# Kernel optimization log

Measured on AMD Instinct MI355X. Metric: run time of the kernel, lower is better.

## Reference

```python
import jax, jax.numpy as jnp
import numpy as np

B, S, N_ITEMS, E, H, L, DFF = 32, 512, 2048, 512, 8, 2, 2048
DK = E // H
EPS = 1e-5


def setup_inputs() -> dict:
    key = jax.random.key(0)
    ks = jax.random.split(key, 32)
    sc = 0.02
    p = {
        'input_seq': jax.random.normal(ks[0], (B, S, N_ITEMS), jnp.float32),
        'emb_W': jax.random.normal(ks[1], (N_ITEMS, E), jnp.float32) * sc,
        'emb_b': jnp.zeros((E,), jnp.float32),
        'pos_emb': jax.random.normal(ks[2], (S, E), jnp.float32) * sc,
        'Wq': jax.random.normal(ks[3], (L, E, E), jnp.float32) * sc,
        'bq': jnp.zeros((L, E), jnp.float32),
        'Wk': jax.random.normal(ks[4], (L, E, E), jnp.float32) * sc,
        'bk': jnp.zeros((L, E), jnp.float32),
        'Wv': jax.random.normal(ks[5], (L, E, E), jnp.float32) * sc,
        'bv': jnp.zeros((L, E), jnp.float32),
        'Wo': jax.random.normal(ks[6], (L, E, E), jnp.float32) * sc,
        'bo': jnp.zeros((L, E), jnp.float32),
        'ln1_g': jnp.ones((L, E), jnp.float32),
        'ln1_b': jnp.zeros((L, E), jnp.float32),
        'W1': jax.random.normal(ks[7], (L, E, DFF), jnp.float32) * sc,
        'b1': jnp.zeros((L, DFF), jnp.float32),
        'W2': jax.random.normal(ks[8], (L, DFF, E), jnp.float32) * sc,
        'b2': jnp.zeros((L, E), jnp.float32),
        'ln2_g': jnp.ones((L, E), jnp.float32),
        'ln2_b': jnp.zeros((L, E), jnp.float32),
        'fc_W': jax.random.normal(ks[9], (E, 1), jnp.float32) * sc,
        'fc_b': jnp.zeros((1,), jnp.float32),
    }
    return p


def _layernorm(x, g, b):
    m = jnp.mean(x, axis=-1, keepdims=True)
    v = jnp.mean(jnp.square(x - m), axis=-1, keepdims=True)
    return (x - m) * jax.lax.rsqrt(v + EPS) * g + b


def reference(input_seq, emb_W, emb_b, pos_emb, Wq, bq, Wk, bk, Wv, bv, Wo, bo,
              ln1_g, ln1_b, W1, b1, W2, b2, ln2_g, ln2_b, fc_W, fc_b):
    x = input_seq @ emb_W + emb_b          # [B,S,E]
    x = x + pos_emb[None, :, :]
    tril = jnp.tril(jnp.ones((S, S), jnp.float32))  # causal lower-triangular
    for l in range(L):
        # --- self attention (faithful: tril BEFORE scale, zeros not -inf) ---
        q = (x @ Wq[l] + bq[l]).reshape(B, S, H, DK).transpose(0, 2, 1, 3)
        k = (x @ Wk[l] + bk[l]).reshape(B, S, H, DK).transpose(0, 2, 1, 3)
        v = (x @ Wv[l] + bv[l]).reshape(B, S, H, DK).transpose(0, 2, 1, 3)
        scores = jnp.einsum('bhqd,bhkd->bhqk', q, k)
        scores = (scores * tril) / np.sqrt(DK)
        probs = jax.nn.softmax(scores, axis=-1)
        attn = jnp.einsum('bhqk,bhkd->bhqd', probs, v)  # [B,H,S,DK]
        attn = attn.transpose(0, 2, 1, 3).reshape(B, S, E)
        attn = attn @ Wo[l] + bo[l]
        # faithful source bug: `self_attention(x,x,x)[0]` -> batch 0 only,
        # broadcast over all batches in the residual add
        attended0 = attn[0]                 # [S,E]
        x = _layernorm(x + attended0[None, :, :], ln1_g[l], ln1_b[l])
        # --- feed forward ---
        ff = jax.nn.relu(x @ W1[l] + b1[l]) @ W2[l] + b2[l]
        x = _layernorm(x + ff, ln2_g[l], ln2_b[l])
    out = (x @ fc_W + fc_b).squeeze(-1)     # [B,S]
    return out
```

## Files before the change

kernel.cpp:

```cpp
#include <hip/hip_runtime.h>


typedef __bf16 bf16;
typedef __bf16 bf16x8 __attribute__((ext_vector_type(8)));
typedef __bf16 bf16x4 __attribute__((ext_vector_type(4)));
typedef float  f32x4  __attribute__((ext_vector_type(4)));

#define SEQ 512

__device__ __forceinline__ void gl2lds16(const bf16* g, void* l) {
    __builtin_amdgcn_global_load_lds(
        (const __attribute__((address_space(1))) void*)g,
        (__attribute__((address_space(3))) void*)l, 16, 0, 0);
}

template<int N> __device__ __forceinline__ void waitvm() {
    if constexpr (N == 0)      asm volatile("s_waitcnt vmcnt(0)" ::: "memory");
    else if constexpr (N == 2) asm volatile("s_waitcnt vmcnt(2)" ::: "memory");
    else if constexpr (N == 3) asm volatile("s_waitcnt vmcnt(3)" ::: "memory");
    else if constexpr (N == 4) asm volatile("s_waitcnt vmcnt(4)" ::: "memory");
    else if constexpr (N == 5) asm volatile("s_waitcnt vmcnt(5)" ::: "memory");
    else if constexpr (N == 6) asm volatile("s_waitcnt vmcnt(6)" ::: "memory");
    else if constexpr (N == 8) asm volatile("s_waitcnt vmcnt(8)" ::: "memory");
    else static_assert(N == 0, "unsupported waitvm");
}

__global__ __launch_bounds__(256)
void cvt_k(const float* __restrict__ in, bf16* __restrict__ outb)
{
    const long long gsz = (long long)gridDim.x * 256;
    const long long n8 = 16384ll * 2048 / 8;
    long long i = (long long)blockIdx.x * 256 + threadIdx.x;
    for (; i + 3 * gsz < n8; i += 4 * gsz) {
        f32x4 a0 = *(const f32x4*)(in + i * 8);
        f32x4 b0 = *(const f32x4*)(in + i * 8 + 4);
        f32x4 a1 = *(const f32x4*)(in + (i + gsz) * 8);
        f32x4 b1 = *(const f32x4*)(in + (i + gsz) * 8 + 4);
        f32x4 a2 = *(const f32x4*)(in + (i + 2 * gsz) * 8);
        f32x4 b2 = *(const f32x4*)(in + (i + 2 * gsz) * 8 + 4);
        f32x4 a3 = *(const f32x4*)(in + (i + 3 * gsz) * 8);
        f32x4 b3 = *(const f32x4*)(in + (i + 3 * gsz) * 8 + 4);
        bf16x8 w0, w1, w2, w3;
        #pragma unroll
        for (int j = 0; j < 4; ++j) {
            w0[j] = (bf16)a0[j]; w0[4 + j] = (bf16)b0[j];
            w1[j] = (bf16)a1[j]; w1[4 + j] = (bf16)b1[j];
            w2[j] = (bf16)a2[j]; w2[4 + j] = (bf16)b2[j];
            w3[j] = (bf16)a3[j]; w3[4 + j] = (bf16)b3[j];
        }
        *(bf16x8*)(outb + i * 8)             = w0;
        *(bf16x8*)(outb + (i + gsz) * 8)     = w1;
        *(bf16x8*)(outb + (i + 2 * gsz) * 8) = w2;
        *(bf16x8*)(outb + (i + 3 * gsz) * 8) = w3;
    }
    for (; i < n8; i += gsz) {
        f32x4 a0 = *(const f32x4*)(in + i * 8);
        f32x4 b0 = *(const f32x4*)(in + i * 8 + 4);
        bf16x8 w0;
        #pragma unroll
        for (int j = 0; j < 4; ++j) { w0[j] = (bf16)a0[j]; w0[4 + j] = (bf16)b0[j]; }
        *(bf16x8*)(outb + i * 8) = w0;
    }
}

__global__ __launch_bounds__(256)
void wtall_k(const float* __restrict__ emb_W, bf16* __restrict__ embWT,
             const float* __restrict__ Wq, const float* __restrict__ Wk,
             const float* __restrict__ Wv, const float* __restrict__ Wo,
             const float* __restrict__ W1, const float* __restrict__ W2,
             bf16* __restrict__ qkvWT, bf16* __restrict__ WoT,
             bf16* __restrict__ W1T, bf16* __restrict__ W2T,
             const float* __restrict__ bq, const float* __restrict__ bk,
             const float* __restrict__ bv, float* __restrict__ qkvB)
{
    const int b = blockIdx.x;
    if (b < 7168) {
        const float* src;
        bf16* dst;
        int K, N, t;
        if (b < 1024) {
            src = emb_W; dst = embWT; K = 2048; N = 512; t = b;
        } else {
            const int bb = b - 1024;
            const int l = bb >= 3072 ? 1 : 0;
            const int r = bb - l * 3072;
            if (r < 256)       { src = Wq + l * 262144;  dst = qkvWT + l * 786432;          K = 512;  N = 512;  t = r; }
            else if (r < 512)  { src = Wk + l * 262144;  dst = qkvWT + l * 786432 + 262144; K = 512;  N = 512;  t = r - 256; }
            else if (r < 768)  { src = Wv + l * 262144;  dst = qkvWT + l * 786432 + 524288; K = 512;  N = 512;  t = r - 512; }
            else if (r < 1024) { src = Wo + l * 262144;  dst = WoT + l * 262144;            K = 512;  N = 512;  t = r - 768; }
            else if (r < 2048) { src = W1 + l * 1048576; dst = W1T + l * 1048576;           K = 512;  N = 2048; t = r - 1024; }
            else               { src = W2 + l * 1048576; dst = W2T + l * 1048576;           K = 2048; N = 512;  t = r - 2048; }
        }
        const int tx = N >> 5;
        const int n0 = (t % tx) * 32, k0 = (t / tx) * 32;
        __shared__ float tl[32][33];
        int r2 = threadIdx.x >> 3, c4 = (threadIdx.x & 7) * 4;
        float4 v = *(const float4*)&src[(long long)(k0 + r2) * N + n0 + c4];
        tl[r2][c4 + 0] = v.x; tl[r2][c4 + 1] = v.y;
        tl[r2][c4 + 2] = v.z; tl[r2][c4 + 3] = v.w;
        __syncthreads();
        int n = threadIdx.x >> 3, kk4 = (threadIdx.x & 7) * 4;
        bf16x4 o;
        o[0] = (bf16)tl[kk4 + 0][n]; o[1] = (bf16)tl[kk4 + 1][n];
        o[2] = (bf16)tl[kk4 + 2][n]; o[3] = (bf16)tl[kk4 + 3][n];
        *(bf16x4*)&dst[(long long)(n0 + n) * K + k0 + kk4] = o;
    } else {
        const int l = b - 7168;
        for (int t2 = threadIdx.x; t2 < 512; t2 += 256) {
            qkvB[l * 1536 + t2]        = bq[l * 512 + t2];
            qkvB[l * 1536 + 512 + t2]  = bk[l * 512 + t2];
            qkvB[l * 1536 + 1024 + t2] = bv[l * 512 + t2];
        }
    }
}

__global__ __launch_bounds__(512, 1)
void fattn(const bf16* __restrict__ qkv,
           const bf16* __restrict__ VT,
           bf16* __restrict__ attn0b)
{
    __shared__ __align__(1024) char smem[65536 + 65536 + 8192];
    char* Ks = smem;
    char* Vs = smem + 65536;
    const int h = blockIdx.y;
    const int q0 = blockIdx.x * 128;
    const int tid = threadIdx.x, lane = tid & 63, wv = tid >> 6;
    const int fr = lane & 15, fc = lane >> 4;
    char* Ps = smem + 131072 + wv * 1024;

    {
        const bf16* Kg = qkv + 512 + h * 64;
        #pragma unroll
        for (int p = 0; p < 8; ++p) {
            int row = p * 64 + (tid >> 3);
            int ch  = tid & 7;
            gl2lds16(Kg + (long long)row * 1536 + ((ch ^ (row & 7)) * 8),
                     Ks + p * 8192 + tid * 16);
        }
        const bf16* Vg = VT + (long long)h * 64 * 512;
        #pragma unroll
        for (int p = 0; p < 8; ++p) {
            int row = p * 8 + (tid >> 6);
            int ch  = tid & 63;
            int chg = (ch & ~7) | ((ch & 7) ^ (row & 7));
            gl2lds16(Vg + (long long)row * 512 + chg * 8,
                     Vs + p * 8192 + tid * 16);
        }
    }
    const int q0w = q0 + wv * 16;
    const int qg  = q0w + fr;
    bf16x8 qf[2];
    #pragma unroll
    for (int w = 0; w < 2; ++w)
        qf[w] = *(const bf16x8*)(qkv + (long long)qg * 1536 + h * 64 + w * 32 + fc * 8);

    asm volatile("s_waitcnt vmcnt(0)" ::: "memory");
    __builtin_amdgcn_s_barrier();
    asm volatile("" ::: "memory");

    f32x4 s[32] = {};
    #pragma unroll
    for (int kt = 0; kt < 32; ++kt) {
        #pragma unroll
        for (int w = 0; w < 2; ++w) {
            int row = kt * 16 + fr;
            bf16x8 kf = *(const bf16x8*)(Ks + row * 128 +
                                         (((w * 4 + fc) ^ (row & 7)) * 16));
            s[kt] = __builtin_amdgcn_mfma_f32_16x16x32_bf16(kf, qf[w], s[kt], 0, 0, 0);
        }
    }

    float mx = -3.4e38f;
    #pragma unroll
    for (int kt = 0; kt < 32; ++kt)
        #pragma unroll
        for (int rr = 0; rr < 4; ++rr) {
            int k = kt * 16 + fc * 4 + rr;
            float v = (k <= qg) ? s[kt][rr] * 0.125f : 0.0f;
            s[kt][rr] = v;
            mx = fmaxf(mx, v);
        }
    mx = fmaxf(mx, __shfl_xor(mx, 16));
    mx = fmaxf(mx, __shfl_xor(mx, 32));
    float sum = 0.f;
    #pragma unroll
    for (int kt = 0; kt < 32; ++kt)
        #pragma unroll
        for (int rr = 0; rr < 4; ++rr) {
            float e = __expf(s[kt][rr] - mx);
            s[kt][rr] = e;
            sum += e;
        }
    sum += __shfl_xor(sum, 16);
    sum += __shfl_xor(sum, 32);
    const float inv = 1.0f / sum;

    f32x4 o[4] = {};
    #pragma unroll
    for (int kt2 = 0; kt2 < 16; ++kt2) {
        bf16x4 u0, u1;
        #pragma unroll
        for (int rr = 0; rr < 4; ++rr) {
            u0[rr] = (bf16)(s[2 * kt2][rr] * inv);
            u1[rr] = (bf16)(s[2 * kt2 + 1][rr] * inv);
        }
        *(bf16x4*)(Ps + fr * 64 + ((fc ^ (fr & 7)) * 8))       = u0;
        *(bf16x4*)(Ps + fr * 64 + (((4 + fc) ^ (fr & 7)) * 8)) = u1;
        __threadfence_block();
        bf16x4 lo = *(const bf16x4*)(Ps + fr * 64 + (((2 * fc) ^ (fr & 7)) * 8));
        bf16x4 hi = *(const bf16x4*)(Ps + fr * 64 + (((2 * fc + 1) ^ (fr & 7)) * 8));
        bf16x8 pf;
        pf[0] = lo[0]; pf[1] = lo[1]; pf[2] = lo[2]; pf[3] = lo[3];
        pf[4] = hi[0]; pf[5] = hi[1]; pf[6] = hi[2]; pf[7] = hi[3];
        #pragma unroll
        for (int n = 0; n < 4; ++n) {
            int row = n * 16 + fr;
            int ch  = kt2 * 4 + fc;
            int chs = (ch & ~7) | ((ch & 7) ^ (row & 7));
            bf16x8 vf = *(const bf16x8*)(Vs + row * 1024 + chs * 16);
            o[n] = __builtin_amdgcn_mfma_f32_16x16x32_bf16(pf, vf, o[n], 0, 0, 0);
        }
    }

    #pragma unroll
    for (int n = 0; n < 4; ++n)
        #pragma unroll
        for (int rr = 0; rr < 4; ++rr) {
            int qrow = q0w + fc * 4 + rr;
            attn0b[(long long)qrow * 512 + h * 64 + n * 16 + fr] = (bf16)o[n][rr];
        }
}

template<int BN, int ACT, int POS>
__global__ __launch_bounds__(512, 1)
void mg8(const bf16* __restrict__ Ab, int lda,
         const bf16* __restrict__ Bt, int ldb,
         const float* __restrict__ bias, const float* __restrict__ pos,
         bf16* __restrict__ Cb, int ldc, int K)
{
    constexpr int BM = 256;
    constexpr int APASS = 2;
    constexpr int BPASS = BN / 128;
    constexpr int AHB = BM * 64;
    constexpr int BHB = BN * 64;
    constexpr int WM = (BN == 256 ? 2 : 4), WN = 8 / WM;
    constexpr int MR = BM / WM / 16;
    constexpr int NR = BN / WN / 16;
    __shared__ __align__(1024) char smem[4 * AHB + 4 * BHB];
    char* ABase = smem;
    char* BBase = smem + 4 * AHB;

    const int gx = gridDim.x, gy = gridDim.y;
    const int nwg = gx * gy;
    const int b = blockIdx.y * gx + blockIdx.x;
    const int q = nwg >> 3, r = nwg & 7;
    const int xcd = b & 7, loc = b >> 3;
    const int wg = (xcd < r ? xcd * (q + 1) : r * (q + 1) + (xcd - r) * q) + loc;
    const int bx = wg % gx, by = wg / gx;
    const int row0 = by * BM, col0 = bx * BN;

    const int tid = threadIdx.x, lane = tid & 63, wv = tid >> 6;
    const int wr = (WM == 2 ? (wv >> 2) : (wv >> 1));
    const int wc = (WM == 2 ? (wv & 3) : (wv & 1));
    const int fr = lane & 15, fc = lane >> 4;

    const bf16* aS[APASS];
    #pragma unroll
    for (int p = 0; p < APASS; ++p) {
        int cL = p * 512 + tid;
        int row = cL >> 2, ch = cL & 3;
        aS[p] = Ab + (long long)(row0 + row) * lda + ((ch ^ (row & 3)) * 8);
    }
    const bf16* bS[BPASS];
    #pragma unroll
    for (int p = 0; p < BPASS; ++p) {
        int cL = p * 512 + tid;
        int row = cL >> 2, ch = cL & 3;
        bS[p] = Bt + (long long)(col0 + row) * ldb + ((ch ^ (row & 3)) * 8);
    }
    int aOff[MR], bOff[NR];
    #pragma unroll
    for (int m = 0; m < MR; ++m) {
        int row = wr * (BM / WM) + m * 16 + fr;
        aOff[m] = row * 64 + ((fc ^ (row & 3)) * 16);
    }
    #pragma unroll
    for (int n = 0; n < NR; ++n) {
        int row = wc * (BN / WN) + n * 16 + fr;
        bOff[n] = row * 64 + ((fc ^ (row & 3)) * 16);
    }

    auto stagePart = [&](int j) {
        const int tau = j >> 2, kh = (j >> 1) & 1, d = tau & 1;
        const int koff = tau * 64 + kh * 32;
        if (!(j & 1)) {
            char* dst = ABase + (d * 2 + kh) * AHB + wv * 1024;
            #pragma unroll
            for (int p = 0; p < APASS; ++p)
                gl2lds16(aS[p] + koff, dst + p * 8192);
        } else {
            char* dst = BBase + (d * 2 + kh) * BHB + wv * 1024;
            #pragma unroll
            for (int p = 0; p < BPASS; ++p)
                gl2lds16(bS[p] + koff, dst + p * 8192);
        }
    };

    const int nt = K >> 6;
    const int T = 4 * nt;
    #pragma unroll
    for (int j = 0; j < 6; ++j)
        if (j < T) stagePart(j);
    waitvm<2 * (APASS + BPASS)>();
    __builtin_amdgcn_s_barrier();

    f32x4 acc[MR][NR] = {};
    const int NPH = 2 * nt;
    for (int g = 0; g < NPH; ++g) {
        const int tau = g >> 1, ks = g & 1, d = tau & 1;

        const char* as = ABase + (d * 2 + ks) * AHB;
        const char* bs = BBase + (d * 2 + ks) * BHB;
        bf16x8 a[MR], b2[NR];
        #pragma unroll
        for (int m = 0; m < MR; ++m) a[m] = *(const bf16x8*)(as + aOff[m]);
        #pragma unroll
        for (int n = 0; n < NR; ++n) b2[n] = *(const bf16x8*)(bs + bOff[n]);

        if (2 * g + 6 < T) stagePart(2 * g + 6);
        if (2 * g + 7 < T) stagePart(2 * g + 7);

        __builtin_amdgcn_s_setprio(1);
        #pragma unroll
        for (int m = 0; m < MR; ++m)
            #pragma unroll
            for (int n = 0; n < NR; ++n)
                acc[m][n] = __builtin_amdgcn_mfma_f32_16x16x32_bf16(
                    a[m], b2[n], acc[m][n], 0, 0, 0);
        __builtin_amdgcn_s_setprio(0);

        const int rem = T - (2 * g + 4);
        if (rem >= 4)      waitvm<2 * (APASS + BPASS)>();
        else if (rem == 3) waitvm<2 * APASS + BPASS>();
        else if (rem == 2) waitvm<APASS + BPASS>();
        else if (rem == 1) waitvm<APASS>();
        else               waitvm<0>();
        __builtin_amdgcn_s_barrier();
    }

    float* st = (float*)(smem + wv * 4096);
    const int rowb = row0 + wr * (BM / WM);
    const int colb = col0 + wc * (BN / WN);
    #pragma unroll
    for (int m = 0; m < MR; ++m) {
        #pragma unroll
        for (int n = 0; n < NR; ++n) {
            int col = colb + n * 16 + fr;
            float bb = bias ? bias[col] : 0.f;
            #pragma unroll
            for (int rr = 0; rr < 4; ++rr) {
                float x = acc[m][n][rr] + bb;
                if constexpr (POS) {
                    int rowg = rowb + m * 16 + fc * 4 + rr;
                    x += pos[(rowg & 511) * 512 + col];
                }
                if constexpr (ACT) x = fmaxf(x, 0.f);
                st[(fc * 4 + rr) * 64 + n * 16 + fr] = x;
            }
        }
        #pragma unroll
        for (int sgi = 0; sgi < 2; ++sgi) {
            int row = sgi * 8 + (lane >> 3);
            int c8 = (lane & 7) * 8;
            f32x4 u = *(const f32x4*)&st[row * 64 + c8];
            f32x4 v = *(const f32x4*)&st[row * 64 + c8 + 4];
            bf16x8 w8;
            w8[0] = (bf16)u[0]; w8[1] = (bf16)u[1];
            w8[2] = (bf16)u[2]; w8[3] = (bf16)u[3];
            w8[4] = (bf16)v[0]; w8[5] = (bf16)v[1];
            w8[6] = (bf16)v[2]; w8[7] = (bf16)v[3];
            *(bf16x8*)&Cb[(long long)(rowb + m * 16 + row) * ldc + colb + c8] = w8;
        }
    }
}

template<int BM, int BN, int ACT, int CMODE, int CAUSAL>
__global__ __launch_bounds__(256, 4)
void mgemm(const bf16* __restrict__ Ab, int lda, long long sA,
           const bf16* __restrict__ Bt, int ldb, long long sB,
           const float* __restrict__ bias,
           float* __restrict__ Cf, bf16* __restrict__ Cb, int ldc, long long sC,
           int K)
{
    static_assert(BM == 128 && (BN == 128 || BN == 64), "tile");
    const int gx = gridDim.x, gy = gridDim.y;
    const int nwg = gx * gy;
    const int b = blockIdx.y * gx + blockIdx.x;
    const int q = nwg >> 3, r = nwg & 7;
    const int xcd = b & 7, loc = b >> 3;
    const int wg = (xcd < r ? xcd * (q + 1) : r * (q + 1) + (xcd - r) * q) + loc;
    const int bx = wg % gx, by = wg / gx;
    if (CAUSAL && bx * BN > by * BM + (BM - 1)) return;

    constexpr int TM = BM / 32, TN = BN / 32;
    constexpr int AIT = BM / 64, BIT = BN / 64;
    constexpr int ABY = BM * 64;
    constexpr int BBY = BN * 64;
    __shared__ bf16 As[2 * BM * 32];
    __shared__ bf16 Bs[2 * BN * 32];
    char* AsB = (char*)As;
    char* BsB = (char*)Bs;
    const int tid = threadIdx.x;
    const int lane = tid & 63, wv = tid >> 6;
    const int wr = wv >> 1, wc = wv & 1;
    const int fr = lane & 15, fc = lane >> 4;
    const int row0 = by * BM, col0 = bx * BN;
    const int z = blockIdx.z;

    Ab += (long long)z * sA;
    Bt += (long long)z * sB;
    if constexpr (CMODE == 0) Cf += (long long)z * sC;
    else                      Cb += (long long)z * sC;

    f32x4 acc[TM][TN] = {};

    const bf16* aSrc[AIT];
    #pragma unroll
    for (int it = 0; it < AIT; ++it) {
        int cL = it * 256 + tid;
        int row = cL >> 2, ch = cL & 3;
        aSrc[it] = Ab + (long long)(row0 + row) * lda + ((ch ^ (row & 3)) * 8);
    }
    const bf16* bSrc[BIT];
    #pragma unroll
    for (int it = 0; it < BIT; ++it) {
        int cL = it * 256 + tid;
        int row = cL >> 2, ch = cL & 3;
        bSrc[it] = Bt + (long long)(col0 + row) * ldb + ((ch ^ (row & 3)) * 8);
    }
    int aOff[TM], bOff[TN];
    #pragma unroll
    for (int m = 0; m < TM; ++m) {
        int row = wr * (BM / 2) + m * 16 + fr;
        aOff[m] = row * 64 + ((fc ^ (row & 3)) * 16);
    }
    #pragma unroll
    for (int n = 0; n < TN; ++n) {
        int row = wc * (BN / 2) + n * 16 + fr;
        bOff[n] = row * 64 + ((fc ^ (row & 3)) * 16);
    }

    auto stageTo = [&](int buf, int kt) {
        #pragma unroll
        for (int it = 0; it < AIT; ++it)
            gl2lds16(aSrc[it] + kt, AsB + buf * ABY + it * 4096 + wv * 1024);
        #pragma unroll
        for (int it = 0; it < BIT; ++it)
            gl2lds16(bSrc[it] + kt, BsB + buf * BBY + it * 4096 + wv * 1024);
    };

    const int nt = K >> 5;
    stageTo(0, 0);
    asm volatile("s_waitcnt vmcnt(0)" ::: "memory");
    __builtin_amdgcn_s_barrier();
    asm volatile("" ::: "memory");

    int cur = 0;
    for (int t = 0; t < nt; ++t) {
        if (t + 1 < nt) stageTo(cur ^ 1, (t + 1) * 32);
        bf16x8 a[TM], b2[TN];
        #pragma unroll
        for (int m = 0; m < TM; ++m) a[m] = *(const bf16x8*)(AsB + cur * ABY + aOff[m]);
        #pragma unroll
        for (int n = 0; n < TN; ++n) b2[n] = *(const bf16x8*)(BsB + cur * BBY + bOff[n]);
        __builtin_amdgcn_s_setprio(1);
        #pragma unroll
        for (int m = 0; m < TM; ++m)
            #pragma unroll
            for (int n = 0; n < TN; ++n)
                acc[m][n] = __builtin_amdgcn_mfma_f32_16x16x32_bf16(a[m], b2[n], acc[m][n], 0, 0, 0);
        __builtin_amdgcn_s_setprio(0);
        if (t + 1 < nt) {
            asm volatile("s_waitcnt vmcnt(0)" ::: "memory");
            __builtin_amdgcn_s_barrier();
            asm volatile("" ::: "memory");
            cur ^= 1;
        }
    }

    #pragma unroll
    for (int n = 0; n < TN; ++n) {
        int col = col0 + wc * (BN / 2) + n * 16 + fr;
        float bb = bias ? bias[col] : 0.f;
        #pragma unroll
        for (int m = 0; m < TM; ++m) {
            int rbase = row0 + wr * (BM / 2) + m * 16 + fc * 4;
            #pragma unroll
            for (int rr = 0; rr < 4; ++rr) {
                float x = acc[m][n][rr] + bb;
                if constexpr (ACT) x = fmaxf(x, 0.f);
                long long ci = (long long)(rbase + rr) * ldc + col;
                if constexpr (CMODE == 0) Cf[ci] = x;
                else                      Cb[ci] = (bf16)x;
            }
        }
    }
}

__global__ __launch_bounds__(256)
void vt_k(const bf16* __restrict__ qkv, bf16* __restrict__ VT)
{
    __shared__ bf16 t[64][80];
    int h = blockIdx.y, s0 = blockIdx.x * 64;
    int r = threadIdx.x >> 2, c16 = (threadIdx.x & 3) * 16;
    const bf16* src = qkv + (long long)(s0 + r) * 1536 + 1024 + h * 64 + c16;
    *(bf16x8*)&t[r][c16]     = *(const bf16x8*)src;
    *(bf16x8*)&t[r][c16 + 8] = *(const bf16x8*)(src + 8);
    __syncthreads();
    int d = r, seg = c16;
    bf16 tmp[16];
    #pragma unroll
    for (int j = 0; j < 16; ++j) tmp[j] = t[seg + j][d];
    bf16* dst = VT + ((long long)(h * 64 + d)) * 512 + s0 + seg;
    *(bf16x8*)dst       = *(bf16x8*)&tmp[0];
    *(bf16x8*)(dst + 8) = *(bf16x8*)&tmp[8];
}

__global__ __launch_bounds__(128)
void addln_k(bf16* __restrict__ xb, const bf16* __restrict__ res,
             unsigned resMask, const float* __restrict__ g,
             const float* __restrict__ bta)
{
    long long row = blockIdx.x;
    int tid = threadIdx.x;
    int c = tid * 4;
    bf16x4 xv4 = *(const bf16x4*)&xb[row * 512 + c];
    bf16x4 rv4 = *(const bf16x4*)&res[(long long)(blockIdx.x & resMask) * 512 + c];
    float x0 = (float)xv4[0] + (float)rv4[0];
    float x1 = (float)xv4[1] + (float)rv4[1];
    float x2 = (float)xv4[2] + (float)rv4[2];
    float x3 = (float)xv4[3] + (float)rv4[3];
    float s = x0 + x1 + x2 + x3;
    float qq = x0 * x0 + x1 * x1 + x2 * x2 + x3 * x3;
    #pragma unroll
    for (int off = 32; off; off >>= 1) {
        s += __shfl_xor(s, off);
        qq += __shfl_xor(qq, off);
    }
    __shared__ float rs[2], rq[2];
    if ((tid & 63) == 0) { rs[tid >> 6] = s; rq[tid >> 6] = qq; }
    __syncthreads();
    s = rs[0] + rs[1]; qq = rq[0] + rq[1];
    float mean = s * (1.0f / 512.0f);
    float var  = qq * (1.0f / 512.0f) - mean * mean;
    float rstd = rsqrtf(var + 1e-5f);
    float4 gv = *(const float4*)&g[c];
    float4 bv = *(const float4*)&bta[c];
    bf16x4 o4;
    o4[0] = (bf16)((x0 - mean) * rstd * gv.x + bv.x);
    o4[1] = (bf16)((x1 - mean) * rstd * gv.y + bv.y);
    o4[2] = (bf16)((x2 - mean) * rstd * gv.z + bv.z);
    o4[3] = (bf16)((x3 - mean) * rstd * gv.w + bv.w);
    *(bf16x4*)&xb[row * 512 + c] = o4;
}

__global__ __launch_bounds__(256)
void fc_k(const bf16* __restrict__ x, const float* __restrict__ w,
          const float* __restrict__ bb, float* __restrict__ out)
{
    int row  = blockIdx.x * 4 + (threadIdx.x >> 6);
    int lane = threadIdx.x & 63;
    const bf16* xr = x + (long long)row * 512;
    bf16x8 a8 = *(const bf16x8*)&xr[lane * 8];
    float4 w0 = *(const float4*)&w[lane * 8];
    float4 w1 = *(const float4*)&w[lane * 8 + 4];
    float s = (float)a8[0] * w0.x + (float)a8[1] * w0.y
            + (float)a8[2] * w0.z + (float)a8[3] * w0.w
            + (float)a8[4] * w1.x + (float)a8[5] * w1.y
            + (float)a8[6] * w1.z + (float)a8[7] * w1.w;
    #pragma unroll
    for (int off = 32; off; off >>= 1) s += __shfl_xor(s, off);
    if (lane == 0) out[row] = s + bb[0];
}

extern "C" void kernel_launch(void* const* d_in, const int* in_sizes, int n_in,
                              void* d_out, int out_size, void* d_ws, size_t ws_size,
                              hipStream_t stream)
{
    const float* input_seq = (const float*)d_in[0];
    const float* emb_W  = (const float*)d_in[1];
    const float* emb_b  = (const float*)d_in[2];
    const float* pos_emb= (const float*)d_in[3];
    const float* Wq = (const float*)d_in[4];
    const float* bq = (const float*)d_in[5];
    const float* Wk = (const float*)d_in[6];
    const float* bk = (const float*)d_in[7];
    const float* Wv = (const float*)d_in[8];
    const float* bv = (const float*)d_in[9];
    const float* Wo = (const float*)d_in[10];
    const float* bo = (const float*)d_in[11];
    const float* ln1_g = (const float*)d_in[12];
    const float* ln1_b = (const float*)d_in[13];
    const float* W1 = (const float*)d_in[14];
    const float* b1 = (const float*)d_in[15];
    const float* W2 = (const float*)d_in[16];
    const float* b2 = (const float*)d_in[17];
    const float* ln2_g = (const float*)d_in[18];
    const float* ln2_b = (const float*)d_in[19];
    const float* fcW = (const float*)d_in[20];
    const float* fcb = (const float*)d_in[21];
    float* out = (float*)d_out;

    char* w = (char*)d_ws;
    size_t off = 0;
    auto alloc = [&](size_t bytes) -> void* {
        off = (off + 255) & ~(size_t)255;
        void* p = w + off;
        off += bytes;
        return p;
    };
    bf16*  xb     = (bf16*) alloc(16384ull * 512 * 2);
    bf16*  embWT  = (bf16*) alloc(512ull * 2048 * 2);
    bf16*  qkvWT  = (bf16*) alloc(2ull * 1536 * 512 * 2);
    bf16*  WoT    = (bf16*) alloc(2ull * 512 * 512 * 2);
    bf16*  W1T    = (bf16*) alloc(2ull * 2048 * 512 * 2);
    bf16*  W2T    = (bf16*) alloc(2ull * 512 * 2048 * 2);
    float* qkvB   = (float*)alloc(2ull * 1536 * 4);
    off = (off + 255) & ~(size_t)255;
    char* dynp = w + off;
    bf16*  seqb     = (bf16*)dynp;
    bf16*  qkv      = (bf16*)dynp;
    bf16*  VT       = (bf16*)(dynp + 1572864);
    bf16*  attn0b   = (bf16*)(dynp + 1572864 + 524288);
    bf16*  attnout0b= (bf16*)(dynp + 1572864 + 524288 + 524288);
    bf16*  hidden = (bf16*)dynp;
    bf16*  ffout  = (bf16*)(dynp + 16384ull * 2048 * 2);

    dim3 blk(256);
    dim3 blk512(512);

    cvt_k<<<dim3(1024), blk, 0, stream>>>(input_seq, seqb);
    wtall_k<<<dim3(7170), blk, 0, stream>>>(
        emb_W, embWT, Wq, Wk, Wv, Wo, W1, W2,
        qkvWT, WoT, W1T, W2T, bq, bk, bv, qkvB);

    mg8<128, 0, 1><<<dim3(4, 64), blk512, 0, stream>>>(
        seqb, 2048, embWT, 2048, emb_b, pos_emb, xb, 512, 2048);

    for (int l = 0; l < 2; ++l) {
        const bf16* qkvWT_l = qkvWT + l * 786432;
        const bf16* WoT_l   = WoT + l * 262144;
        const bf16* W1T_l   = W1T + l * 1048576;
        const bf16* W2T_l   = W2T + l * 1048576;

        mgemm<128, 64, 0, 1, 0><<<dim3(24, 4), blk, 0, stream>>>(
            xb, 512, 0, qkvWT_l, 512, 0, qkvB + l * 1536,
            nullptr, qkv, 1536, 0, 512);
        vt_k<<<dim3(8, 8), blk, 0, stream>>>(qkv, VT);
        fattn<<<dim3(4, 8), blk512, 0, stream>>>(qkv, VT, attn0b);
        mgemm<128, 64, 0, 1, 0><<<dim3(8, 4), blk, 0, stream>>>(
            attn0b, 512, 0, WoT_l, 512, 0, bo + l * 512, nullptr,
            attnout0b, 512, 0, 512);
        addln_k<<<dim3(16384), dim3(128), 0, stream>>>(
            xb, attnout0b, 511u, ln1_g + l * 512, ln1_b + l * 512);

        mg8<256, 1, 0><<<dim3(8, 64), blk512, 0, stream>>>(
            xb, 512, W1T_l, 512, b1 + l * 2048, nullptr, hidden, 2048, 512);
        mg8<128, 0, 0><<<dim3(4, 64), blk512, 0, stream>>>(
            hidden, 2048, W2T_l, 2048, b2 + l * 512, nullptr, ffout, 512, 2048);
        addln_k<<<dim3(16384), dim3(128), 0, stream>>>(
            xb, ffout, 0xffffffffu, ln2_g + l * 512, ln2_b + l * 512);
    }

    fc_k<<<dim3(4096), blk, 0, stream>>>(xb, fcW, fcb, out);
}
```

Measured before the change: 366.0 us.

## Merge prep kernels, split attention into smaller blocks, two rows per layernorm block

Fuses the input conversion and weight transpose kernels into one launch, which saves a kernel launch and lets the two kinds of work overlap. Attention blocks now cover 64 query rows with 4 waves, doubling the grid from 32 to 64 blocks so more CUs are used; each block still loads the full K and V for its head into LDS, so total K/V traffic doubles. The add+layernorm kernel now handles two rows per 256-thread block, halving the number of blocks.

```diff
diff --git a/kernel.cpp b/kernel.cpp
--- a/kernel.cpp
+++ b/kernel.cpp
@@ -26,55 +26,53 @@
 }
 
 __global__ __launch_bounds__(256)
-void cvt_k(const float* __restrict__ in, bf16* __restrict__ outb)
-{
-    const long long gsz = (long long)gridDim.x * 256;
-    const long long n8 = 16384ll * 2048 / 8;
-    long long i = (long long)blockIdx.x * 256 + threadIdx.x;
-    for (; i + 3 * gsz < n8; i += 4 * gsz) {
-        f32x4 a0 = *(const f32x4*)(in + i * 8);
-        f32x4 b0 = *(const f32x4*)(in + i * 8 + 4);
-        f32x4 a1 = *(const f32x4*)(in + (i + gsz) * 8);
-        f32x4 b1 = *(const f32x4*)(in + (i + gsz) * 8 + 4);
-        f32x4 a2 = *(const f32x4*)(in + (i + 2 * gsz) * 8);
-        f32x4 b2 = *(const f32x4*)(in + (i + 2 * gsz) * 8 + 4);
-        f32x4 a3 = *(const f32x4*)(in + (i + 3 * gsz) * 8);
-        f32x4 b3 = *(const f32x4*)(in + (i + 3 * gsz) * 8 + 4);
-        bf16x8 w0, w1, w2, w3;
-        #pragma unroll
-        for (int j = 0; j < 4; ++j) {
-            w0[j] = (bf16)a0[j]; w0[4 + j] = (bf16)b0[j];
-            w1[j] = (bf16)a1[j]; w1[4 + j] = (bf16)b1[j];
-            w2[j] = (bf16)a2[j]; w2[4 + j] = (bf16)b2[j];
-            w3[j] = (bf16)a3[j]; w3[4 + j] = (bf16)b3[j];
-        }
-        *(bf16x8*)(outb + i * 8)             = w0;
-        *(bf16x8*)(outb + (i + gsz) * 8)     = w1;
-        *(bf16x8*)(outb + (i + 2 * gsz) * 8) = w2;
-        *(bf16x8*)(outb + (i + 3 * gsz) * 8) = w3;
-    }
-    for (; i < n8; i += gsz) {
-        f32x4 a0 = *(const f32x4*)(in + i * 8);
-        f32x4 b0 = *(const f32x4*)(in + i * 8 + 4);
-        bf16x8 w0;
-        #pragma unroll
-        for (int j = 0; j < 4; ++j) { w0[j] = (bf16)a0[j]; w0[4 + j] = (bf16)b0[j]; }
-        *(bf16x8*)(outb + i * 8) = w0;
-    }
-}
-
-__global__ __launch_bounds__(256)
-void wtall_k(const float* __restrict__ emb_W, bf16* __restrict__ embWT,
-             const float* __restrict__ Wq, const float* __restrict__ Wk,
-             const float* __restrict__ Wv, const float* __restrict__ Wo,
-             const float* __restrict__ W1, const float* __restrict__ W2,
-             bf16* __restrict__ qkvWT, bf16* __restrict__ WoT,
-             bf16* __restrict__ W1T, bf16* __restrict__ W2T,
-             const float* __restrict__ bq, const float* __restrict__ bk,
-             const float* __restrict__ bv, float* __restrict__ qkvB)
-{
-    const int b = blockIdx.x;
-    if (b < 7168) {
+void prep_k(const float* __restrict__ in, bf16* __restrict__ outb,
+            const float* __restrict__ emb_W, bf16* __restrict__ embWT,
+            const float* __restrict__ Wq, const float* __restrict__ Wk,
+            const float* __restrict__ Wv, const float* __restrict__ Wo,
+            const float* __restrict__ W1, const float* __restrict__ W2,
+            bf16* __restrict__ qkvWT, bf16* __restrict__ WoT,
+            bf16* __restrict__ W1T, bf16* __restrict__ W2T,
+            const float* __restrict__ bq, const float* __restrict__ bk,
+            const float* __restrict__ bv, float* __restrict__ qkvB)
+{
+    const int blk = blockIdx.x;
+    if (blk < 1024) {
+        const long long gsz = 1024ll * 256;
+        const long long n8 = 16384ll * 2048 / 8;
+        long long i = (long long)blk * 256 + threadIdx.x;
+        for (; i + 3 * gsz < n8; i += 4 * gsz) {
+            f32x4 a0 = *(const f32x4*)(in + i * 8);
+            f32x4 b0 = *(const f32x4*)(in + i * 8 + 4);
+            f32x4 a1 = *(const f32x4*)(in + (i + gsz) * 8);
+            f32x4 b1 = *(const f32x4*)(in + (i + gsz) * 8 + 4);
+            f32x4 a2 = *(const f32x4*)(in + (i + 2 * gsz) * 8);
+            f32x4 b2 = *(const f32x4*)(in + (i + 2 * gsz) * 8 + 4);
+            f32x4 a3 = *(const f32x4*)(in + (i + 3 * gsz) * 8);
+            f32x4 b3 = *(const f32x4*)(in + (i + 3 * gsz) * 8 + 4);
+            bf16x8 w0, w1, w2, w3;
+            #pragma unroll
+            for (int j = 0; j < 4; ++j) {
+                w0[j] = (bf16)a0[j]; w0[4 + j] = (bf16)b0[j];
+                w1[j] = (bf16)a1[j]; w1[4 + j] = (bf16)b1[j];
+                w2[j] = (bf16)a2[j]; w2[4 + j] = (bf16)b2[j];
+                w3[j] = (bf16)a3[j]; w3[4 + j] = (bf16)b3[j];
+            }
+            *(bf16x8*)(outb + i * 8)             = w0;
+            *(bf16x8*)(outb + (i + gsz) * 8)     = w1;
+            *(bf16x8*)(outb + (i + 2 * gsz) * 8) = w2;
+            *(bf16x8*)(outb + (i + 3 * gsz) * 8) = w3;
+        }
+        for (; i < n8; i += gsz) {
+            f32x4 a0 = *(const f32x4*)(in + i * 8);
+            f32x4 b0 = *(const f32x4*)(in + i * 8 + 4);
+            bf16x8 w0;
+            #pragma unroll
+            for (int j = 0; j < 4; ++j) { w0[j] = (bf16)a0[j]; w0[4 + j] = (bf16)b0[j]; }
+            *(bf16x8*)(outb + i * 8) = w0;
+        }
+    } else if (blk < 8192) {
+        const int b = blk - 1024;
         const float* src;
         bf16* dst;
         int K, N, t;
@@ -105,7 +103,7 @@
         o[2] = (bf16)tl[kk4 + 2][n]; o[3] = (bf16)tl[kk4 + 3][n];
         *(bf16x4*)&dst[(long long)(n0 + n) * K + k0 + kk4] = o;
     } else {
-        const int l = b - 7168;
+        const int l = blk - 8192;
         for (int t2 = threadIdx.x; t2 < 512; t2 += 256) {
             qkvB[l * 1536 + t2]        = bq[l * 512 + t2];
             qkvB[l * 1536 + 512 + t2]  = bk[l * 512 + t2];
@@ -114,16 +112,16 @@
     }
 }
 
-__global__ __launch_bounds__(512, 1)
+__global__ __launch_bounds__(256, 1)
 void fattn(const bf16* __restrict__ qkv,
            const bf16* __restrict__ VT,
            bf16* __restrict__ attn0b)
 {
-    __shared__ __align__(1024) char smem[65536 + 65536 + 8192];
+    __shared__ __align__(1024) char smem[65536 + 65536 + 4096];
     char* Ks = smem;
     char* Vs = smem + 65536;
     const int h = blockIdx.y;
-    const int q0 = blockIdx.x * 128;
+    const int q0 = blockIdx.x * 64;
     const int tid = threadIdx.x, lane = tid & 63, wv = tid >> 6;
     const int fr = lane & 15, fc = lane >> 4;
     char* Ps = smem + 131072 + wv * 1024;
@@ -131,20 +129,20 @@
     {
         const bf16* Kg = qkv + 512 + h * 64;
         #pragma unroll
-        for (int p = 0; p < 8; ++p) {
-            int row = p * 64 + (tid >> 3);
+        for (int p = 0; p < 16; ++p) {
+            int row = p * 32 + (tid >> 3);
             int ch  = tid & 7;
             gl2lds16(Kg + (long long)row * 1536 + ((ch ^ (row & 7)) * 8),
-                     Ks + p * 8192 + tid * 16);
+                     Ks + p * 4096 + tid * 16);
         }
         const bf16* Vg = VT + (long long)h * 64 * 512;
         #pragma unroll
-        for (int p = 0; p < 8; ++p) {
-            int row = p * 8 + (tid >> 6);
+        for (int p = 0; p < 16; ++p) {
+            int row = p * 4 + (tid >> 6);
             int ch  = tid & 63;
             int chg = (ch & ~7) | ((ch & 7) ^ (row & 7));
             gl2lds16(Vg + (long long)row * 512 + chg * 8,
-                     Vs + p * 8192 + tid * 16);
+                     Vs + p * 4096 + tid * 16);
         }
     }
     const int q0w = q0 + wv * 16;
@@ -526,16 +524,18 @@
     *(bf16x8*)(dst + 8) = *(bf16x8*)&tmp[8];
 }
 
-__global__ __launch_bounds__(128)
+__global__ __launch_bounds__(256)
 void addln_k(bf16* __restrict__ xb, const bf16* __restrict__ res,
              unsigned resMask, const float* __restrict__ g,
              const float* __restrict__ bta)
 {
-    long long row = blockIdx.x;
-    int tid = threadIdx.x;
-    int c = tid * 4;
+    const int tid = threadIdx.x;
+    const int sub = tid >> 7;
+    const long long row = (long long)blockIdx.x * 2 + sub;
+    const int lt = tid & 127;
+    const int c = lt * 4;
     bf16x4 xv4 = *(const bf16x4*)&xb[row * 512 + c];
-    bf16x4 rv4 = *(const bf16x4*)&res[(long long)(blockIdx.x & resMask) * 512 + c];
+    bf16x4 rv4 = *(const bf16x4*)&res[(long long)(row & resMask) * 512 + c];
     float x0 = (float)xv4[0] + (float)rv4[0];
     float x1 = (float)xv4[1] + (float)rv4[1];
     float x2 = (float)xv4[2] + (float)rv4[2];
@@ -547,10 +547,11 @@
         s += __shfl_xor(s, off);
         qq += __shfl_xor(qq, off);
     }
-    __shared__ float rs[2], rq[2];
+    __shared__ float rs[4], rq[4];
     if ((tid & 63) == 0) { rs[tid >> 6] = s; rq[tid >> 6] = qq; }
     __syncthreads();
-    s = rs[0] + rs[1]; qq = rq[0] + rq[1];
+    s = rs[sub * 2] + rs[sub * 2 + 1];
+    qq = rq[sub * 2] + rq[sub * 2 + 1];
     float mean = s * (1.0f / 512.0f);
     float var  = qq * (1.0f / 512.0f) - mean * mean;
     float rstd = rsqrtf(var + 1e-5f);
@@ -639,9 +640,8 @@
     dim3 blk(256);
     dim3 blk512(512);
 
-    cvt_k<<<dim3(1024), blk, 0, stream>>>(input_seq, seqb);
-    wtall_k<<<dim3(7170), blk, 0, stream>>>(
-        emb_W, embWT, Wq, Wk, Wv, Wo, W1, W2,
+    prep_k<<<dim3(8194), blk, 0, stream>>>(
+        input_seq, seqb, emb_W, embWT, Wq, Wk, Wv, Wo, W1, W2,
         qkvWT, WoT, W1T, W2T, bq, bk, bv, qkvB);
 
     mg8<128, 0, 1><<<dim3(4, 64), blk512, 0, stream>>>(
@@ -657,18 +657,18 @@
             xb, 512, 0, qkvWT_l, 512, 0, qkvB + l * 1536,
             nullptr, qkv, 1536, 0, 512);
         vt_k<<<dim3(8, 8), blk, 0, stream>>>(qkv, VT);
-        fattn<<<dim3(4, 8), blk512, 0, stream>>>(qkv, VT, attn0b);
+        fattn<<<dim3(8, 8), blk, 0, stream>>>(qkv, VT, attn0b);
         mgemm<128, 64, 0, 1, 0><<<dim3(8, 4), blk, 0, stream>>>(
             attn0b, 512, 0, WoT_l, 512, 0, bo + l * 512, nullptr,
             attnout0b, 512, 0, 512);
-        addln_k<<<dim3(16384), dim3(128), 0, stream>>>(
+        addln_k<<<dim3(8192), blk, 0, stream>>>(
             xb, attnout0b, 511u, ln1_g + l * 512, ln1_b + l * 512);
 
         mg8<256, 1, 0><<<dim3(8, 64), blk512, 0, stream>>>(
             xb, 512, W1T_l, 512, b1 + l * 2048, nullptr, hidden, 2048, 512);
         mg8<128, 0, 0><<<dim3(4, 64), blk512, 0, stream>>>(
             hidden, 2048, W2T_l, 2048, b2 + l * 512, nullptr, ffout, 512, 2048);
-        addln_k<<<dim3(16384), dim3(128), 0, stream>>>(
+        addln_k<<<dim3(8192), blk, 0, stream>>>(
             xb, ffout, 0xffffffffu, ln2_g + l * 512, ln2_b + l * 512);
     }
 
```

After: 362.4 us. About the same (-1.0%).
